# Kernel tuning notes

Measured on AMD Instinct MI355X. Metric: run time of the kernel, lower is better.

## Reference

```python
import jax, jax.numpy as jnp
import numpy as np

B, TQ, TP, D = 4, 512, 512, 256


def setup_inputs() -> dict:
    key = jax.random.key(0)
    ks = jax.random.split(key, 5)
    return {
        "q": jax.random.normal(ks[0], (B, TQ, D), dtype=jnp.float32),
        "p": jax.random.normal(ks[1], (B, TP, D), dtype=jnp.float32),
        "W0": jax.random.normal(ks[2], (D, D), dtype=jnp.float32) / np.sqrt(D),
        "W1": jax.random.normal(ks[3], (D, D), dtype=jnp.float32) / np.sqrt(D),
        "vc": jax.random.normal(ks[4], (D, 1), dtype=jnp.float32) * 0.05,
    }


def reference(q, p, W0, W1, vc):
    # q: [B,Tq,Dq], p: [B,Tp,Dp]
    prod_q = jnp.einsum('bqd,de->bqe', q, W0)   # [B,Tq,dim]
    prod_p = jnp.einsum('bpd,de->bpe', p, W1)   # [B,Tp,dim]
    # additive attention energies: tanh over broadcast sum [B,Tp,Tq,dim]
    energy = jnp.tanh(prod_p[:, :, None, :] + prod_q[:, None, :, :])
    scores = jnp.einsum('bpqe,e->bpq', energy, vc[:, 0])  # [B,Tp,Tq]
    # original softmax is over axis=-2 of [B,Tp,Tq], i.e. the Tp axis
    weights = jax.nn.softmax(scores, axis=1)   # [B,Tp,Tq]
    # weighted sum over the Tq axis of (tiled) q
    attention_q = jnp.einsum('bpq,bqd->bpd', weights, q)  # [B,Tp,Dq]
    return attention_q
```

## Files before the change

### kernel.cpp

```cpp
#include <hip/hip_runtime.h>

#define NB 4
#define TT 512
#define DD 256
#define K2L2E    2.885390081777927f
#define NEG2L2E (-2.885390081777927f)

#if defined(__has_builtin)
# if __has_builtin(__builtin_amdgcn_global_load_lds)
#  define HAS_GLL 1
# endif
#endif

typedef float v2f __attribute__((ext_vector_type(2)));

__device__ __forceinline__ v2f pk_fma(v2f a, v2f b, v2f c) {
#if defined(__has_builtin)
# if __has_builtin(__builtin_elementwise_fma)
    return __builtin_elementwise_fma(a, b, c);
# else
    v2f r; r.x = __builtin_fmaf(a.x, b.x, c.x); r.y = __builtin_fmaf(a.y, b.y, c.y); return r;
# endif
#else
    v2f r; r.x = __builtin_fmaf(a.x, b.x, c.x); r.y = __builtin_fmaf(a.y, b.y, c.y); return r;
#endif
}
__device__ __forceinline__ v2f splat2(float s) { v2f r; r.x = s; r.y = s; return r; }

__device__ __forceinline__ void stage16(const float* __restrict__ g, float* l) {
#ifdef HAS_GLL
    __builtin_amdgcn_global_load_lds((const __attribute__((address_space(1))) void*)g,
                                     (__attribute__((address_space(3))) void*)l, 16, 0, 0);
#else
    *(float4*)l = *(const float4*)g;
#endif
}

__global__ __launch_bounds__(256) void proj_exp_kernel(
    const float* __restrict__ qin, const float* __restrict__ pin,
    const float* __restrict__ W0, const float* __restrict__ W1,
    float* __restrict__ expQ, float* __restrict__ expP)
{
    const int blk = blockIdx.x;
    const int wh = blk >> 8, tid = blk & 255;
    const int m0 = (tid >> 2) * 32, n0 = (tid & 3) * 64;
    const float* A = wh ? pin : qin;
    const float* W = wh ? W1 : W0;
    float* OUT     = wh ? expP : expQ;

    __shared__ __align__(16) float As[32 * 34];
    __shared__ __align__(16) float Bs[32 * 64];

    const int t  = threadIdx.x;
    const int ar = t >> 3, ac4 = (t & 7) * 4;
    const int br = t >> 4, bc4 = (t & 15) * 4;
    const int tn = t >> 4, tm = t & 15;

    const float* Ap = A + (long)(m0 + ar) * DD + ac4;

    float4 av  = *(const float4*)Ap;
    float4 bv0 = *(const float4*)(W + (long)br * DD + n0 + bc4);
    float4 bv1 = *(const float4*)(W + (long)(br + 16) * DD + n0 + bc4);

    float acc[2][4] = {};

    for (int c = 0; c < 8; ++c) {
        As[(ac4 + 0) * 34 + ar] = av.x;
        As[(ac4 + 1) * 34 + ar] = av.y;
        As[(ac4 + 2) * 34 + ar] = av.z;
        As[(ac4 + 3) * 34 + ar] = av.w;
        *(float4*)&Bs[br * 64 + bc4]        = bv0;
        *(float4*)&Bs[(br + 16) * 64 + bc4] = bv1;
        __syncthreads();
        if (c < 7) {
            int k1 = (c + 1) * 32;
            av  = *(const float4*)(Ap + k1);
            bv0 = *(const float4*)(W + (long)(k1 + br) * DD + n0 + bc4);
            bv1 = *(const float4*)(W + (long)(k1 + 16 + br) * DD + n0 + bc4);
        }
        #pragma unroll
        for (int kk = 0; kk < 32; ++kk) {
            float2 a = *(const float2*)&As[kk * 34 + 2 * tm];
            float4 b = *(const float4*)&Bs[kk * 64 + 4 * tn];
            float aa[2] = {a.x, a.y};
            float bb[4] = {b.x, b.y, b.z, b.w};
            #pragma unroll
            for (int i = 0; i < 2; ++i)
                #pragma unroll
                for (int j = 0; j < 4; ++j)
                    acc[i][j] = __builtin_fmaf(aa[i], bb[j], acc[i][j]);
        }
        __syncthreads();
    }

    const int  bi = m0 >> 9;
    const int  ml = (m0 & 511) + 2 * tm;
    #pragma unroll
    for (int j = 0; j < 4; ++j) {
        int d = n0 + 4 * tn + j;
        float2 st;
        st.x = __builtin_amdgcn_exp2f(acc[0][j] * K2L2E);
        st.y = __builtin_amdgcn_exp2f(acc[1][j] * K2L2E);
        *(float2*)(OUT + ((long)bi * DD + d) * TT + ml) = st;
    }
}

__global__ __launch_bounds__(512, 4) void score_kernel(
    const float* __restrict__ expP, const float* __restrict__ expQ,
    const float* __restrict__ vc, float* __restrict__ ebuf, float* __restrict__ lpart)
{
    const int b = blockIdx.z, pt = blockIdx.y, qt = blockIdx.x;
    const int p0 = pt * 32, q0 = qt * 64;
    const int t  = threadIdx.x;
    const int qx = t & 31, py = t >> 5;

    __shared__ __align__(16) float PA[2][64 * 32];
    __shared__ __align__(16) float QB[2][64 * 64];
    __shared__ float vcs[DD];

    const float* gP = expP + (long)b * DD * TT + p0;
    const float* gQ = expQ + (long)b * DD * TT + q0;

    {
        int d = t >> 3, off = (t & 7) * 4;
        stage16(gP + (long)d * TT + off, &PA[0][t * 4]);
    }
    #pragma unroll
    for (int s = 0; s < 2; ++s) {
        int f = t + 512 * s, d = f >> 4, off = (f & 15) * 4;
        stage16(gQ + (long)d * TT + off, &QB[0][f * 4]);
    }
    if (t < DD) vcs[t] = vc[t];
    __syncthreads();

    v2f acc[2]; acc[0] = splat2(0.f); acc[1] = splat2(0.f);

    for (int c = 0; c < 4; ++c) {
        if (c < 3) {
            int dc = (c + 1) * 64, nb = (c + 1) & 1;
            {
                int d = t >> 3, off = (t & 7) * 4;
                stage16(gP + (long)(dc + d) * TT + off, &PA[nb][t * 4]);
            }
            #pragma unroll
            for (int s = 0; s < 2; ++s) {
                int f = t + 512 * s, d = f >> 4, off = (f & 15) * 4;
                stage16(gQ + (long)(dc + d) * TT + off, &QB[nb][f * 4]);
            }
        }
        const float* PAc = PA[c & 1];
        const float* QBc = QB[c & 1];
        const float* vcb = &vcs[c * 64];
        #pragma unroll 8
        for (int dp = 0; dp < 32; ++dp) {
            float2 vp = *(const float2*)&vcb[2 * dp];
            v2f vsv = splat2(vp.x + vp.y);
            v2f vx  = splat2(vp.x), vy = splat2(vp.y);
            float2 A0 = *(const float2*)&PAc[(2 * dp) * 32 + 2 * py];
            float2 A1 = *(const float2*)&PAc[(2 * dp + 1) * 32 + 2 * py];
            v2f B0 = *(const v2f*)&QBc[(2 * dp) * 64 + 2 * qx];
            v2f B1 = *(const v2f*)&QBc[(2 * dp + 1) * 64 + 2 * qx];
            float a0[2] = {A0.x, A0.y}, a1[2] = {A1.x, A1.y};
            #pragma unroll
            for (int i = 0; i < 2; ++i) {
                v2f E0  = splat2(a0[i]) * B0;
                v2f E1  = splat2(a1[i]) * B1;
                v2f u   = (E0 + E1) + 1.0f;
                v2f den = pk_fma(E0, E1, u);
                v2f num = pk_fma(vy, E0, pk_fma(vx, E1, vsv));
                v2f r;
                r.x = __builtin_amdgcn_rcpf(den.x);
                r.y = __builtin_amdgcn_rcpf(den.y);
                acc[i] = pk_fma(num, r, acc[i]);
            }
        }
        __syncthreads();
    }

    float* eb = ebuf + ((long)b * TT + p0) * TT + q0;
    v2f colp = splat2(0.f);
    #pragma unroll
    for (int i = 0; i < 2; ++i) {
        float2 ev;
        ev.x = __builtin_amdgcn_exp2f(acc[i].x * NEG2L2E);
        ev.y = __builtin_amdgcn_exp2f(acc[i].y * NEG2L2E);
        *(float2*)(eb + (long)(2 * py + i) * TT + 2 * qx) = ev;
        colp.x += ev.x; colp.y += ev.y;
    }
    float* scr = (float*)&PA[0][0];
    *(float2*)&scr[py * 64 + 2 * qx] = make_float2(colp.x, colp.y);
    __syncthreads();
    if (t < 64) {
        float s = 0.f;
        #pragma unroll
        for (int r = 0; r < 16; ++r) s += scr[r * 64 + t];
        lpart[((long)b * 16 + pt) * TT + q0 + t] = s;
    }
}

__global__ __launch_bounds__(128) void out_kernel(
    const float* __restrict__ ebuf, const float* __restrict__ qin,
    const float* __restrict__ lpart, float* __restrict__ out)
{
    const int b = blockIdx.z, pt = blockIdx.y, dt = blockIdx.x;
    const int m0 = pt * 32, n0 = dt * 32;
    const int t  = threadIdx.x;
    const int tm = t >> 4;
    const int tn = t & 15;

    __shared__ __align__(16) float As[64 * 36];
    __shared__ __align__(16) float Bs[64 * 36];
    __shared__ float linv[TT];

    #pragma unroll
    for (int s = 0; s < 4; ++s) {
        int qq = t + 128 * s;
        float sum = 0.f;
        #pragma unroll
        for (int pb = 0; pb < 16; ++pb) sum += lpart[((long)b * 16 + pb) * TT + qq];
        linv[qq] = __builtin_amdgcn_rcpf(sum);
    }
    __syncthreads();

    const float* Ab = ebuf + ((long)b * TT + m0) * TT;
    const float* Bb = qin + (long)b * TT * DD + n0;

    const int ar  = t >> 2;
    const int akc = (t & 3) * 4;
    const int brr = t >> 3;
    const int bc4 = (t & 7) * 4;

    float4 av[4], bv[4];
    #pragma unroll
    for (int u = 0; u < 4; ++u) {
        av[u] = *(const float4*)(Ab + (long)ar * TT + 16 * u + akc);
        bv[u] = *(const float4*)(Bb + (long)(brr + 16 * u) * DD + bc4);
    }

    v2f acc[4]; acc[0] = splat2(0.f); acc[1] = splat2(0.f);
    acc[2] = splat2(0.f); acc[3] = splat2(0.f);

    for (int c = 0; c < 8; ++c) {
        const int k0 = c * 64;
        #pragma unroll
        for (int u = 0; u < 4; ++u) {
            int kl = 16 * u + akc;
            As[(kl + 0) * 36 + ar] = av[u].x;
            As[(kl + 1) * 36 + ar] = av[u].y;
            As[(kl + 2) * 36 + ar] = av[u].z;
            As[(kl + 3) * 36 + ar] = av[u].w;
            float s = linv[k0 + brr + 16 * u];
            float4 w;
            w.x = bv[u].x * s; w.y = bv[u].y * s; w.z = bv[u].z * s; w.w = bv[u].w * s;
            *(float4*)&Bs[(brr + 16 * u) * 36 + bc4] = w;
        }
        __syncthreads();
        if (c < 7) {
            int k1 = (c + 1) * 64;
            #pragma unroll
            for (int u = 0; u < 4; ++u) {
                av[u] = *(const float4*)(Ab + (long)ar * TT + k1 + 16 * u + akc);
                bv[u] = *(const float4*)(Bb + (long)(k1 + brr + 16 * u) * DD + bc4);
            }
        }
        #pragma unroll
        for (int kk = 0; kk < 64; ++kk) {
            float4 a = *(const float4*)&As[kk * 36 + 4 * tm];
            v2f bb = *(const v2f*)&Bs[kk * 36 + 2 * tn];
            acc[0] = pk_fma(splat2(a.x), bb, acc[0]);
            acc[1] = pk_fma(splat2(a.y), bb, acc[1]);
            acc[2] = pk_fma(splat2(a.z), bb, acc[2]);
            acc[3] = pk_fma(splat2(a.w), bb, acc[3]);
        }
        __syncthreads();
    }

    #pragma unroll
    for (int i = 0; i < 4; ++i) {
        *(float2*)(out + ((long)b * TT + m0 + 4 * tm + i) * DD + n0 + 2 * tn) =
            make_float2(acc[i].x, acc[i].y);
    }
}

extern "C" void kernel_launch(void* const* d_in, const int* in_sizes, int n_in,
                              void* d_out, int out_size, void* d_ws, size_t ws_size,
                              hipStream_t stream) {
    const float* q  = (const float*)d_in[0];
    const float* p  = (const float*)d_in[1];
    const float* W0 = (const float*)d_in[2];
    const float* W1 = (const float*)d_in[3];
    const float* vc = (const float*)d_in[4];
    float* out = (float*)d_out;

    float* ws    = (float*)d_ws;
    float* expQ  = ws;
    float* expP  = ws + 524288;
    float* ebuf  = ws + 1048576;
    float* lpart = ws + 2097152;

    proj_exp_kernel<<<dim3(512), 256, 0, stream>>>(q, p, W0, W1, expQ, expP);
    score_kernel<<<dim3(8, 16, NB), 512, 0, stream>>>(expP, expQ, vc, ebuf, lpart);
    out_kernel<<<dim3(8, 16, NB), 128, 0, stream>>>(ebuf, q, lpart, out);
}
```

Baseline: 125.6 us.

## Replace double-buffered 64-d chunks with single-buffered 128-d chunks in score kernel

The score kernel drops its 4-stage double-buffered LDS pipeline over 64-wide D chunks. It now loads two 128-wide D chunks into a single buffer, with an explicit sync before and after the second load. It also raises the launch-bounds occupancy hint from 4 to 6 blocks per CU. This cuts barrier count and per-chunk overhead but removes the overlap between global loads and compute, so the second load is exposed unless other resident blocks hide it. LDS per block stays roughly the same, and the higher occupancy target may force register pressure or spills.

```diff
diff --git a/kernel.cpp b/kernel.cpp
--- a/kernel.cpp
+++ b/kernel.cpp
@@ -105,7 +105,7 @@
     }
 }
 
-__global__ __launch_bounds__(512, 4) void score_kernel(
+__global__ __launch_bounds__(512, 6) void score_kernel(
     const float* __restrict__ expP, const float* __restrict__ expQ,
     const float* __restrict__ vc, float* __restrict__ ebuf, float* __restrict__ lpart)
 {
@@ -114,52 +114,53 @@
     const int t  = threadIdx.x;
     const int qx = t & 31, py = t >> 5;
 
-    __shared__ __align__(16) float PA[2][64 * 32];
-    __shared__ __align__(16) float QB[2][64 * 64];
+    __shared__ __align__(16) float PA[128 * 32];
+    __shared__ __align__(16) float QB[128 * 64];
     __shared__ float vcs[DD];
 
     const float* gP = expP + (long)b * DD * TT + p0;
     const float* gQ = expQ + (long)b * DD * TT + q0;
 
-    {
-        int d = t >> 3, off = (t & 7) * 4;
-        stage16(gP + (long)d * TT + off, &PA[0][t * 4]);
-    }
     #pragma unroll
     for (int s = 0; s < 2; ++s) {
+        int f = t + 512 * s, d = f >> 3, off = (f & 7) * 4;
+        stage16(gP + (long)d * TT + off, &PA[f * 4]);
+    }
+    #pragma unroll
+    for (int s = 0; s < 4; ++s) {
         int f = t + 512 * s, d = f >> 4, off = (f & 15) * 4;
-        stage16(gQ + (long)d * TT + off, &QB[0][f * 4]);
+        stage16(gQ + (long)d * TT + off, &QB[f * 4]);
     }
     if (t < DD) vcs[t] = vc[t];
     __syncthreads();
 
     v2f acc[2]; acc[0] = splat2(0.f); acc[1] = splat2(0.f);
 
-    for (int c = 0; c < 4; ++c) {
-        if (c < 3) {
-            int dc = (c + 1) * 64, nb = (c + 1) & 1;
-            {
-                int d = t >> 3, off = (t & 7) * 4;
-                stage16(gP + (long)(dc + d) * TT + off, &PA[nb][t * 4]);
+    for (int c = 0; c < 2; ++c) {
+        if (c == 1) {
+            __syncthreads();
+            #pragma unroll
+            for (int s = 0; s < 2; ++s) {
+                int f = t + 512 * s, d = f >> 3, off = (f & 7) * 4;
+                stage16(gP + (long)(128 + d) * TT + off, &PA[f * 4]);
             }
             #pragma unroll
-            for (int s = 0; s < 2; ++s) {
+            for (int s = 0; s < 4; ++s) {
                 int f = t + 512 * s, d = f >> 4, off = (f & 15) * 4;
-                stage16(gQ + (long)(dc + d) * TT + off, &QB[nb][f * 4]);
+                stage16(gQ + (long)(128 + d) * TT + off, &QB[f * 4]);
             }
-        }
-        const float* PAc = PA[c & 1];
-        const float* QBc = QB[c & 1];
-        const float* vcb = &vcs[c * 64];
+            __syncthreads();
+        }
+        const float* vcb = &vcs[c * 128];
         #pragma unroll 8
-        for (int dp = 0; dp < 32; ++dp) {
+        for (int dp = 0; dp < 64; ++dp) {
             float2 vp = *(const float2*)&vcb[2 * dp];
             v2f vsv = splat2(vp.x + vp.y);
             v2f vx  = splat2(vp.x), vy = splat2(vp.y);
-            float2 A0 = *(const float2*)&PAc[(2 * dp) * 32 + 2 * py];
-            float2 A1 = *(const float2*)&PAc[(2 * dp + 1) * 32 + 2 * py];
-            v2f B0 = *(const v2f*)&QBc[(2 * dp) * 64 + 2 * qx];
-            v2f B1 = *(const v2f*)&QBc[(2 * dp + 1) * 64 + 2 * qx];
+            float2 A0 = *(const float2*)&PA[(2 * dp) * 32 + 2 * py];
+            float2 A1 = *(const float2*)&PA[(2 * dp + 1) * 32 + 2 * py];
+            v2f B0 = *(const v2f*)&QB[(2 * dp) * 64 + 2 * qx];
+            v2f B1 = *(const v2f*)&QB[(2 * dp + 1) * 64 + 2 * qx];
             float a0[2] = {A0.x, A0.y}, a1[2] = {A1.x, A1.y};
             #pragma unroll
             for (int i = 0; i < 2; ++i) {
@@ -174,7 +175,6 @@
                 acc[i] = pk_fma(num, r, acc[i]);
             }
         }
-        __syncthreads();
     }
 
     float* eb = ebuf + ((long)b * TT + p0) * TT + q0;
@@ -187,7 +187,8 @@
         *(float2*)(eb + (long)(2 * py + i) * TT + 2 * qx) = ev;
         colp.x += ev.x; colp.y += ev.y;
     }
-    float* scr = (float*)&PA[0][0];
+    __syncthreads();
+    float* scr = (float*)&PA[0];
     *(float2*)&scr[py * 64 + 2 * qx] = make_float2(colp.x, colp.y);
     __syncthreads();
     if (t < 64) {
```

Result: no change. 124.4 us (-1.0%).
